# Kernel tuning notes

Measured on AMD Instinct MI355X. Metric: run time of the kernel, lower is better.

Reference implementation:

```python
import jax, jax.numpy as jnp
import numpy as np

N_ATOMS = 200000   # total atoms in batch
N_NBR   = 10       # max neighbors per atom (a2a width)
N_MOLS  = 8000     # molecules in batch (25 atoms each)
HID     = 128      # hidden_size
FDIM    = 151      # raw atom feature dim (GROVER default)
FEAT    = 200      # molecule-level descriptor dim
DFF     = 4 * HID  # PositionwiseFeedForward inner dim
FFN_H   = 256      # mol_atom_from_atom_ffn hidden
TASKS   = 12       # num_tasks
EPS     = 1e-6     # GROVER LayerNorm eps


def setup_inputs() -> dict:
    key = jax.random.key(0)
    ks = jax.random.split(key, 14)
    s = 0.02
    atoms_per_mol = N_ATOMS // N_MOLS
    starts = (jnp.arange(N_MOLS, dtype=jnp.int32) * atoms_per_mol)
    sizes = jnp.full((N_MOLS,), atoms_per_mol, dtype=jnp.int32)
    a_scope = jnp.stack([starts, sizes], axis=1)  # [M, 2]
    return {
        "atom_output": jax.random.normal(ks[0], (N_ATOMS, HID), jnp.float32),
        "original_f_atoms": jax.random.normal(ks[1], (N_ATOMS, FDIM), jnp.float32),
        "features_batch": jax.random.normal(ks[2], (N_MOLS, FEAT), jnp.float32),
        "a2a": jax.random.randint(ks[3], (N_ATOMS, N_NBR), 0, N_ATOMS, jnp.int32),
        "a_scope": a_scope,
        # PositionwiseFeedForward (ffn_atom_from_atom): in = FDIM + HID
        "W1": jax.random.normal(ks[4], (FDIM + HID, DFF), jnp.float32) * s,
        "b1": jnp.zeros((DFF,), jnp.float32),
        "W2": jax.random.normal(ks[5], (DFF, HID), jnp.float32) * s,
        "b2": jnp.zeros((HID,), jnp.float32),
        # SublayerConnection LayerNorm
        "gamma": jnp.ones((HID,), jnp.float32),
        "beta": jnp.zeros((HID,), jnp.float32),
        # mol_atom_from_atom_ffn: in = HID + FEAT
        "Wf1": jax.random.normal(ks[6], (HID + FEAT, FFN_H), jnp.float32) * s,
        "bf1": jnp.zeros((FFN_H,), jnp.float32),
        "Wf2": jax.random.normal(ks[7], (FFN_H, TASKS), jnp.float32) * s,
        "bf2": jnp.zeros((TASKS,), jnp.float32),
    }


def _layernorm(x, gamma, beta):
    mu = jnp.mean(x, axis=-1, keepdims=True)
    var = jnp.mean((x - mu) ** 2, axis=-1, keepdims=True)
    return gamma * (x - mu) * jax.lax.rsqrt(var + EPS) + beta


def reference(atom_output, original_f_atoms, features_batch, a2a, a_scope,
              W1, b1, W2, b2, gamma, beta, Wf1, bf1, Wf2, bf2):
    # select_neighbor_and_aggregate: gather neighbor embeddings, sum over nbrs
    aggr = jnp.sum(atom_output[a2a], axis=1)                      # [N, HID]
    x = jnp.concatenate([original_f_atoms, aggr], axis=1)         # [N, FDIM+HID]
    # PositionwiseFeedForward (eval: dropout = identity)
    h = jax.nn.relu(x @ W1 + b1)
    ffn_out = h @ W2 + b2                                         # [N, HID]
    # SublayerConnection(None, x) -> dropout(LayerNorm(x))
    atom_emb = _layernorm(ffn_out, gamma, beta)                   # [N, HID]
    # Readout: mean-pool per molecule via a_scope (start, size)
    starts = a_scope[:, 0]
    sizes = a_scope[:, 1].astype(atom_emb.dtype)
    seg = jnp.searchsorted(starts, jnp.arange(atom_emb.shape[0], dtype=starts.dtype), side="right") - 1
    mol = jax.ops.segment_sum(atom_emb, seg, num_segments=a_scope.shape[0]) / sizes[:, None]
    # concat molecule descriptors, then mol_atom_from_atom_ffn
    mol = jnp.concatenate([mol, features_batch], axis=1)          # [M, HID+FEAT]
    out = jax.nn.relu(mol @ Wf1 + bf1) @ Wf2 + bf2                # [M, TASKS]
    return out
```

## Files before the change

kernel.cpp:

```cpp
#include <hip/hip_runtime.h>
#include <hip/hip_bf16.h>

#define N_ATOMS 200000
#define N_NBR 10
#define N_MOLS 8000
#define HID 128
#define FDIM 151
#define FEAT 200
#define DFF 512
#define FFN_H 256
#define TASKS 12
#define KX 279
#define K1P 288
#define XSB 288
#define HSB 128
#define FS 132
#define KM 328
#define K3 352
#define MS 360
#define MT 80
#define MI 5
#define SMEM_ATOMS (MT * XSB * 2 + MT * HSB * 2)

typedef __hip_bfloat16 bf16;
typedef __attribute__((ext_vector_type(8))) __bf16 bf16x8;
typedef __attribute__((ext_vector_type(4))) float f32x4;

__device__ __forceinline__ float bf2f(bf16 x) { return __bfloat162float(x); }
__device__ __forceinline__ float blo(unsigned w) { union { unsigned u; float f; } c; c.u = w << 16; return c.f; }
__device__ __forceinline__ float bhi(unsigned w) { union { unsigned u; float f; } c; c.u = w & 0xFFFF0000u; return c.f; }

__device__ __forceinline__ int xswz(int r, int e) {
  return r * XSB + (e ^ ((e < 256 ? (r & 7) : (r & 3)) << 3));
}
__device__ __forceinline__ int hswz(int r, int e) {
  return r * HSB + (e ^ ((r & 7) << 3));
}

__global__ void prep_weights_kernel(const float* __restrict__ W1,
                                    const float* __restrict__ W2,
                                    const float* __restrict__ Wf1,
                                    bf16* __restrict__ W1bT,
                                    bf16* __restrict__ W2bT,
                                    bf16* __restrict__ Wf1bT) {
  int idx = blockIdx.x * 256 + threadIdx.x;
  if (idx < DFF * K1P) {
    int n = idx / K1P, k = idx - n * K1P;
    float v;
    if (k < HID)      v = W1[(size_t)(FDIM + k) * DFF + n];
    else if (k < KX)  v = W1[(size_t)(k - HID) * DFF + n];
    else              v = 0.f;
    W1bT[idx] = __float2bfloat16(v);
    return;
  }
  idx -= DFF * K1P;
  if (idx < HID * DFF) {
    int n = idx / DFF, k = idx - n * DFF;
    W2bT[idx] = __float2bfloat16(W2[(size_t)k * HID + n]);
    return;
  }
  idx -= HID * DFF;
  if (idx < FFN_H * K3) {
    int n = idx / K3, k = idx - n * K3;
    float v = (k < KM) ? Wf1[(size_t)k * FFN_H + n] : 0.f;
    Wf1bT[idx] = __float2bfloat16(v);
  }
}

__global__ void conv_ao_kernel(const float* __restrict__ ao, bf16* __restrict__ ao16) {
  const int idx = blockIdx.x * 256 + threadIdx.x;
  const float4 v0 = *(const float4*)&ao[(size_t)idx * 8];
  const float4 v1 = *(const float4*)&ao[(size_t)idx * 8 + 4];
  union { bf16 h[8]; uint4 u; } pk;
  pk.h[0] = __float2bfloat16(v0.x); pk.h[1] = __float2bfloat16(v0.y);
  pk.h[2] = __float2bfloat16(v0.z); pk.h[3] = __float2bfloat16(v0.w);
  pk.h[4] = __float2bfloat16(v1.x); pk.h[5] = __float2bfloat16(v1.y);
  pk.h[6] = __float2bfloat16(v1.z); pk.h[7] = __float2bfloat16(v1.w);
  *(uint4*)&ao16[(size_t)idx * 8] = pk.u;
}

__global__ __launch_bounds__(256)
void gather_kernel(const bf16* __restrict__ ao16,
                   const int* __restrict__ a2a,
                   bf16* __restrict__ aggr) {
  const int gid = blockIdx.x * 256 + threadIdx.x;
  const int atom = gid >> 4, c8 = gid & 15;
  int idxs[N_NBR];
#pragma unroll
  for (int j = 0; j < N_NBR; ++j) idxs[j] = a2a[atom * N_NBR + j];
  float s[8];
#pragma unroll
  for (int e = 0; e < 8; ++e) s[e] = 0.f;
#pragma unroll
  for (int j = 0; j < N_NBR; ++j) {
    const uint4 u = *(const uint4*)&ao16[(size_t)idxs[j] * HID + c8 * 8];
    s[0] += blo(u.x); s[1] += bhi(u.x);
    s[2] += blo(u.y); s[3] += bhi(u.y);
    s[4] += blo(u.z); s[5] += bhi(u.z);
    s[6] += blo(u.w); s[7] += bhi(u.w);
  }
  union { bf16 h[8]; uint4 u; } pk;
#pragma unroll
  for (int e = 0; e < 8; ++e) pk.h[e] = __float2bfloat16(s[e]);
  *(uint4*)&aggr[(size_t)atom * HID + c8 * 8] = pk.u;
}

__global__ __launch_bounds__(512, 4)
void atoms_kernel(const bf16* __restrict__ aggr,
                  const float* __restrict__ f_atoms,
                  const bf16* __restrict__ W1bT,
                  const float* __restrict__ b1,
                  const bf16* __restrict__ W2bT,
                  const float* __restrict__ b2,
                  const float* __restrict__ gamma,
                  const float* __restrict__ beta,
                  bf16* __restrict__ atom_emb) {
  extern __shared__ char smem[];
  bf16* Xs = (bf16*)smem;
  bf16* Hs = (bf16*)(smem + MT * XSB * 2);
  float* Fs = (float*)smem;

  const int tid = threadIdx.x;
  const int m0 = blockIdx.x * MT;
  const int lane = tid & 63;
  const int w = tid >> 6;
  const int lr = lane & 15;
  const int lk = lane >> 4;

  {
    int q = tid;
#pragma unroll
    for (int p = 0; p < 3; ++p) {
      if (p < 2 || q < MT * 16) {
        const int r = q >> 4, c8 = q & 15;
        *(uint4*)&Xs[r * XSB + ((c8 ^ (r & 7)) << 3)] =
            *(const uint4*)&aggr[(size_t)(m0 + r) * HID + c8 * 8];
      }
      q += 512;
    }
  }
  {
    const float* fb = &f_atoms[(size_t)m0 * FDIM];
    int u = tid;
#pragma unroll
    for (int p = 0; p < 3; ++p) {
      if (p < 2 || u < MT * 19) {
        const int row = u / 19, o = u - row * 19;
        const float* src = &fb[row * FDIM + o * 8];
        float vf[8];
        if (o < 18) {
          const float4 va = *(const float4*)src;
          const float4 vb = *(const float4*)(src + 4);
          vf[0] = va.x; vf[1] = va.y; vf[2] = va.z; vf[3] = va.w;
          vf[4] = vb.x; vf[5] = vb.y; vf[6] = vb.z; vf[7] = vb.w;
        } else {
          const float4 va = *(const float4*)src;
          vf[0] = va.x; vf[1] = va.y; vf[2] = va.z; vf[3] = va.w;
          vf[4] = src[4]; vf[5] = src[5]; vf[6] = src[6]; vf[7] = 0.f;
        }
        union { bf16 h[8]; uint4 q4; } pk;
#pragma unroll
        for (int e = 0; e < 8; ++e) pk.h[e] = __float2bfloat16(vf[e]);
        const int ob = 16 + o;
        const int obs = (ob < 32) ? (ob ^ (row & 7)) : (ob ^ (row & 3));
        *(uint4*)&Xs[row * XSB + obs * 8] = pk.q4;
      }
      u += 512;
    }
  }
  if (tid < MT) {
    const uint4 z = {0u, 0u, 0u, 0u};
    *(uint4*)&Xs[tid * XSB + ((35 ^ (tid & 3)) << 3)] = z;
  }
  __syncthreads();

  f32x4 acc2[MI];
#pragma unroll
  for (int mi = 0; mi < MI; ++mi) acc2[mi] = (f32x4)0.f;

#pragma unroll 1
  for (int pp = 0; pp < 2; ++pp) {
    const int c0 = pp * 2;
    f32x4 acc1[2][MI];
#pragma unroll
    for (int c = 0; c < 2; ++c)
#pragma unroll
      for (int mi = 0; mi < MI; ++mi) acc1[c][mi] = (f32x4)0.f;
    {
      const bf16* w1p = &W1bT[(size_t)(c0 * 128 + w * 16 + lr) * K1P + lk * 8];
      __builtin_amdgcn_s_setprio(1);
#pragma unroll
      for (int kk = 0; kk < K1P / 32; ++kk) {
        const bf16x8 b0 = *(const bf16x8*)&w1p[kk * 32];
        const bf16x8 b1f = *(const bf16x8*)&w1p[(size_t)128 * K1P + kk * 32];
#pragma unroll
        for (int mi = 0; mi < MI; ++mi) {
          const bf16x8 a = *(const bf16x8*)&Xs[xswz(mi * 16 + lr, kk * 32 + lk * 8)];
          acc1[0][mi] = __builtin_amdgcn_mfma_f32_16x16x32_bf16(b0, a, acc1[0][mi], 0, 0, 0);
          acc1[1][mi] = __builtin_amdgcn_mfma_f32_16x16x32_bf16(b1f, a, acc1[1][mi], 0, 0, 0);
        }
      }
      __builtin_amdgcn_s_setprio(0);
    }
#pragma unroll
    for (int c = 0; c < 2; ++c) {
      const int nc = c0 + c;
      {
        const float4 bb = *(const float4*)&b1[nc * 128 + w * 16 + lk * 4];
        const float bbf[4] = { bb.x, bb.y, bb.z, bb.w };
#pragma unroll
        for (int mi = 0; mi < MI; ++mi) {
          union { bf16 h[4]; uint2 u2; } pk;
#pragma unroll
          for (int r = 0; r < 4; ++r) {
            const float h = acc1[c][mi][r] + bbf[r];
            pk.h[r] = __float2bfloat16(h > 0.f ? h : 0.f);
          }
          *(uint2*)&Hs[hswz(mi * 16 + lr, w * 16 + lk * 4)] = pk.u2;
        }
      }
      __syncthreads();
      {
        const bf16* w2p = &W2bT[(size_t)(w * 16 + lr) * DFF + nc * 128 + lk * 8];
        __builtin_amdgcn_s_setprio(1);
#pragma unroll
        for (int kk = 0; kk < 4; ++kk) {
          const bf16x8 wb = *(const bf16x8*)&w2p[kk * 32];
#pragma unroll
          for (int mi = 0; mi < MI; ++mi) {
            const bf16x8 hb = *(const bf16x8*)&Hs[hswz(mi * 16 + lr, kk * 32 + lk * 8)];
            acc2[mi] = __builtin_amdgcn_mfma_f32_16x16x32_bf16(wb, hb, acc2[mi], 0, 0, 0);
          }
        }
        __builtin_amdgcn_s_setprio(0);
      }
      __syncthreads();
    }
  }

  {
    const float4 b2v = *(const float4*)&b2[w * 16 + lk * 4];
#pragma unroll
    for (int mi = 0; mi < MI; ++mi) {
      float4 v;
      v.x = acc2[mi][0] + b2v.x;
      v.y = acc2[mi][1] + b2v.y;
      v.z = acc2[mi][2] + b2v.z;
      v.w = acc2[mi][3] + b2v.w;
      *(float4*)&Fs[(mi * 16 + lr) * FS + w * 16 + lk * 4] = v;
    }
  }
  __syncthreads();

  const float gam0 = gamma[lane], gam1 = gamma[64 + lane];
  const float bet0 = beta[lane],  bet1 = beta[64 + lane];
#pragma unroll
  for (int i = 0; i < MT / 8; ++i) {
    const int row = w * (MT / 8) + i;
    const float x0 = Fs[row * FS + lane];
    const float x1 = Fs[row * FS + 64 + lane];
    float s = x0 + x1;
    float q = x0 * x0 + x1 * x1;
#pragma unroll
    for (int off = 32; off > 0; off >>= 1) {
      s += __shfl_xor(s, off);
      q += __shfl_xor(q, off);
    }
    const float mu = s * (1.f / 128.f);
    const float var = q * (1.f / 128.f) - mu * mu;
    const float rs = rsqrtf(var + 1e-6f);
    const int atom = m0 + row;
    atom_emb[(size_t)atom * HID + lane] =
        __float2bfloat16(gam0 * ((x0 - mu) * rs) + bet0);
    atom_emb[(size_t)atom * HID + 64 + lane] =
        __float2bfloat16(gam1 * ((x1 - mu) * rs) + bet1);
  }
}

__global__ __launch_bounds__(256)
void mol_kernel(const bf16* __restrict__ atom_emb,
                const float* __restrict__ features,
                const int* __restrict__ a_scope,
                bf16* __restrict__ mol_cat) {
  const int tid = threadIdx.x;
  const int mi = tid >> 4, c8 = tid & 15;
  const int base = blockIdx.x * 16;
  const int m = base + mi;
  const int start = a_scope[2 * m];
  const int size  = a_scope[2 * m + 1];
  float s[8];
#pragma unroll
  for (int e = 0; e < 8; ++e) s[e] = 0.f;
  for (int a = 0; a < size; ++a) {
    const uint4 u = *(const uint4*)&atom_emb[(size_t)(start + a) * HID + c8 * 8];
    s[0] += blo(u.x); s[1] += bhi(u.x);
    s[2] += blo(u.y); s[3] += bhi(u.y);
    s[4] += blo(u.z); s[5] += bhi(u.z);
    s[6] += blo(u.w); s[7] += bhi(u.w);
  }
  const float inv = 1.f / (float)size;
  union { bf16 h[8]; uint4 u; } pk;
#pragma unroll
  for (int e = 0; e < 8; ++e) pk.h[e] = __float2bfloat16(s[e] * inv);
  *(uint4*)&mol_cat[(size_t)m * K3 + c8 * 8] = pk.u;
  for (int q = tid; q < 16 * 50; q += 256) {
    const int mm = q / 50, qq = q - mm * 50;
    const float4 v = *(const float4*)&features[(size_t)(base + mm) * FEAT + qq * 4];
    union { bf16 h[4]; uint2 u2; } pf;
    pf.h[0] = __float2bfloat16(v.x); pf.h[1] = __float2bfloat16(v.y);
    pf.h[2] = __float2bfloat16(v.z); pf.h[3] = __float2bfloat16(v.w);
    *(uint2*)&mol_cat[(size_t)(base + mm) * K3 + HID + qq * 4] = pf.u2;
  }
  for (int q = tid; q < 16 * (K3 - KM); q += 256) {
    const int mm = q / (K3 - KM), qq = q - mm * (K3 - KM);
    mol_cat[(size_t)(base + mm) * K3 + KM + qq] = __float2bfloat16(0.f);
  }
}

__global__ __launch_bounds__(512)
void molffn1_kernel(const bf16* __restrict__ mol_cat,
                    const bf16* __restrict__ Wf1bT,
                    const float* __restrict__ bf1,
                    bf16* __restrict__ Hf) {
  __shared__ bf16 As[64 * MS];
  const int tid = threadIdx.x;
  const int m0 = blockIdx.x * 64;
  for (int idx = tid; idx < 64 * (K3 / 8); idx += 512) {
    int rr = idx / (K3 / 8), qv = idx - rr * (K3 / 8);
    *(uint4*)&As[rr * MS + qv * 8] = *(const uint4*)&mol_cat[(size_t)(m0 + rr) * K3 + qv * 8];
  }
  __syncthreads();
  const int lane = tid & 63, w = tid >> 6;
  const int lr = lane & 15, lk = lane >> 4;
  const int wn = w * 32;
  f32x4 acc[4][2];
#pragma unroll
  for (int mi = 0; mi < 4; ++mi)
#pragma unroll
    for (int ni = 0; ni < 2; ++ni) acc[mi][ni] = (f32x4)0.f;
#pragma unroll 3
  for (int kk = 0; kk < K3 / 32; ++kk) {
    bf16x8 a[4], b[2];
#pragma unroll
    for (int mi = 0; mi < 4; ++mi)
      a[mi] = *(const bf16x8*)&As[(mi * 16 + lr) * MS + kk * 32 + lk * 8];
#pragma unroll
    for (int ni = 0; ni < 2; ++ni)
      b[ni] = *(const bf16x8*)&Wf1bT[(size_t)(wn + ni * 16 + lr) * K3 + kk * 32 + lk * 8];
#pragma unroll
    for (int mi = 0; mi < 4; ++mi)
#pragma unroll
      for (int ni = 0; ni < 2; ++ni)
        acc[mi][ni] = __builtin_amdgcn_mfma_f32_16x16x32_bf16(a[mi], b[ni], acc[mi][ni], 0, 0, 0);
  }
#pragma unroll
  for (int ni = 0; ni < 2; ++ni) {
    const int n = wn + ni * 16 + lr;
    const float bias = bf1[n];
#pragma unroll
    for (int mi = 0; mi < 4; ++mi)
#pragma unroll
      for (int rr = 0; rr < 4; ++rr) {
        const int row = mi * 16 + lk * 4 + rr;
        const float h = acc[mi][ni][rr] + bias;
        Hf[(size_t)(m0 + row) * FFN_H + n] = __float2bfloat16(h > 0.f ? h : 0.f);
      }
  }
}

__global__ __launch_bounds__(192)
void molffn2_kernel(const bf16* __restrict__ Hf,
                    const float* __restrict__ Wf2,
                    const float* __restrict__ bias2,
                    float* __restrict__ out) {
  __shared__ float Ws[FFN_H * TASKS];
  const int tid = threadIdx.x;
  for (int i = tid; i < FFN_H * TASKS; i += 192) Ws[i] = Wf2[i];
  __syncthreads();
  const int m = blockIdx.x * 16 + tid / TASKS;
  const int t = tid % TASKS;
  float s = bias2[t];
  for (int k8 = 0; k8 < FFN_H / 8; ++k8) {
    const uint4 u = *(const uint4*)&Hf[(size_t)m * FFN_H + k8 * 8];
    const float h[8] = { blo(u.x), bhi(u.x), blo(u.y), bhi(u.y),
                         blo(u.z), bhi(u.z), blo(u.w), bhi(u.w) };
#pragma unroll
    for (int e = 0; e < 8; ++e) s += h[e] * Ws[(k8 * 8 + e) * TASKS + t];
  }
  out[(size_t)m * TASKS + t] = s;
}

extern "C" void kernel_launch(void* const* d_in, const int* in_sizes, int n_in,
                              void* d_out, int out_size, void* d_ws, size_t ws_size,
                              hipStream_t stream) {
  const float* atom_output = (const float*)d_in[0];
  const float* f_atoms     = (const float*)d_in[1];
  const float* features    = (const float*)d_in[2];
  const int*   a2a         = (const int*)d_in[3];
  const int*   a_scope     = (const int*)d_in[4];
  const float* W1   = (const float*)d_in[5];
  const float* b1   = (const float*)d_in[6];
  const float* W2   = (const float*)d_in[7];
  const float* b2   = (const float*)d_in[8];
  const float* gamma = (const float*)d_in[9];
  const float* beta  = (const float*)d_in[10];
  const float* Wf1  = (const float*)d_in[11];
  const float* bf1  = (const float*)d_in[12];
  const float* Wf2  = (const float*)d_in[13];
  const float* bf2v = (const float*)d_in[14];
  float* out = (float*)d_out;

  char* ws = (char*)d_ws;
  size_t off = 0;
  bf16* W1bT  = (bf16*)(ws + off); off += (size_t)DFF * K1P * 2;
  bf16* W2bT  = (bf16*)(ws + off); off += (size_t)HID * DFF * 2;
  bf16* Wf1bT = (bf16*)(ws + off); off += (size_t)FFN_H * K3 * 2;
  bf16* atom_emb = (bf16*)(ws + off); off += (size_t)N_ATOMS * HID * 2;
  bf16* mol_cat  = (bf16*)(ws + off); off += (size_t)N_MOLS * K3 * 2;
  bf16* Hf       = (bf16*)(ws + off); off += (size_t)N_MOLS * FFN_H * 2;
  bf16* ao16     = (bf16*)(ws + off); off += (size_t)N_ATOMS * HID * 2;
  bf16* aggr = atom_emb;

  hipFuncSetAttribute((const void*)atoms_kernel,
                      hipFuncAttributeMaxDynamicSharedMemorySize, SMEM_ATOMS);

  hipLaunchKernelGGL(prep_weights_kernel, dim3(1184), dim3(256), 0, stream,
                     W1, W2, Wf1, W1bT, W2bT, Wf1bT);
  hipLaunchKernelGGL(conv_ao_kernel, dim3(N_ATOMS * HID / 8 / 256), dim3(256), 0, stream,
                     atom_output, ao16);
  hipLaunchKernelGGL(gather_kernel, dim3(N_ATOMS * 16 / 256), dim3(256), 0, stream,
                     ao16, a2a, aggr);
  hipLaunchKernelGGL(atoms_kernel, dim3(N_ATOMS / MT), dim3(512), SMEM_ATOMS, stream,
                     aggr, f_atoms,
                     W1bT, b1, W2bT, b2, gamma, beta, atom_emb);
  hipLaunchKernelGGL(mol_kernel, dim3(N_MOLS / 16), dim3(256), 0, stream,
                     atom_emb, features, a_scope, mol_cat);
  hipLaunchKernelGGL(molffn1_kernel, dim3(N_MOLS / 64), dim3(512), 0, stream,
                     mol_cat, Wf1bT, bf1, Hf);
  hipLaunchKernelGGL(molffn2_kernel, dim3(N_MOLS / 16), dim3(192), 0, stream,
                     Hf, Wf2, bf2v, out);
}
```

Baseline: 283.6 us.

## Process two atom tiles per block and prefetch next tile's features

The atoms kernel now handles two 80-atom tiles per block, halving the grid. While the first tile's GEMMs run, the second tile's f_atoms rows are loaded into registers, hiding that global load latency. The first GEMM is restructured to compute one 128-column chunk at a time instead of two, which lowers register pressure at the cost of more barriers and fewer independent MFMA chains. A custom barrier waits only on LDS counters, so the outstanding global prefetch is not drained; the halved grid may worsen tail imbalance across CUs.

```diff
diff --git a/kernel.cpp b/kernel.cpp
--- a/kernel.cpp
+++ b/kernel.cpp
@@ -26,6 +26,8 @@
 typedef __attribute__((ext_vector_type(8))) __bf16 bf16x8;
 typedef __attribute__((ext_vector_type(4))) float f32x4;
 
+#define BAR() do { asm volatile("s_waitcnt lgkmcnt(0)" ::: "memory"); __builtin_amdgcn_s_barrier(); } while (0)
+
 __device__ __forceinline__ float bf2f(bf16 x) { return __bfloat162float(x); }
 __device__ __forceinline__ float blo(unsigned w) { union { unsigned u; float f; } c; c.u = w << 16; return c.f; }
 __device__ __forceinline__ float bhi(unsigned w) { union { unsigned u; float f; } c; c.u = w & 0xFFFF0000u; return c.f; }
@@ -121,90 +123,110 @@
   float* Fs = (float*)smem;
 
   const int tid = threadIdx.x;
-  const int m0 = blockIdx.x * MT;
   const int lane = tid & 63;
   const int w = tid >> 6;
   const int lr = lane & 15;
   const int lk = lane >> 4;
+  const int urow = tid / 19;
+  const int uo = tid - urow * 19;
+
+  float4 fa0[3], fa1[3];
 
   {
-    int q = tid;
-#pragma unroll
-    for (int p = 0; p < 3; ++p) {
-      if (p < 2 || q < MT * 16) {
-        const int r = q >> 4, c8 = q & 15;
-        *(uint4*)&Xs[r * XSB + ((c8 ^ (r & 7)) << 3)] =
-            *(const uint4*)&aggr[(size_t)(m0 + r) * HID + c8 * 8];
-      }
-      q += 512;
-    }
-  }
-  {
-    const float* fb = &f_atoms[(size_t)m0 * FDIM];
+    const float* fb = &f_atoms[(size_t)(blockIdx.x * 2) * MT * FDIM];
     int u = tid;
 #pragma unroll
     for (int p = 0; p < 3; ++p) {
       if (p < 2 || u < MT * 19) {
-        const int row = u / 19, o = u - row * 19;
+        const int row = u / 19, o = u - (u / 19) * 19;
         const float* src = &fb[row * FDIM + o * 8];
-        float vf[8];
-        if (o < 18) {
-          const float4 va = *(const float4*)src;
-          const float4 vb = *(const float4*)(src + 4);
-          vf[0] = va.x; vf[1] = va.y; vf[2] = va.z; vf[3] = va.w;
-          vf[4] = vb.x; vf[5] = vb.y; vf[6] = vb.z; vf[7] = vb.w;
-        } else {
-          const float4 va = *(const float4*)src;
-          vf[0] = va.x; vf[1] = va.y; vf[2] = va.z; vf[3] = va.w;
-          vf[4] = src[4]; vf[5] = src[5]; vf[6] = src[6]; vf[7] = 0.f;
-        }
-        union { bf16 h[8]; uint4 q4; } pk;
-#pragma unroll
-        for (int e = 0; e < 8; ++e) pk.h[e] = __float2bfloat16(vf[e]);
-        const int ob = 16 + o;
-        const int obs = (ob < 32) ? (ob ^ (row & 7)) : (ob ^ (row & 3));
-        *(uint4*)&Xs[row * XSB + obs * 8] = pk.q4;
+        fa0[p] = *(const float4*)src;
+        if (o < 18) fa1[p] = *(const float4*)(src + 4);
+        else { fa1[p].x = src[4]; fa1[p].y = src[5]; fa1[p].z = src[6]; fa1[p].w = 0.f; }
       }
       u += 512;
     }
   }
-  if (tid < MT) {
-    const uint4 z = {0u, 0u, 0u, 0u};
-    *(uint4*)&Xs[tid * XSB + ((35 ^ (tid & 3)) << 3)] = z;
-  }
-  __syncthreads();
-
-  f32x4 acc2[MI];
-#pragma unroll
-  for (int mi = 0; mi < MI; ++mi) acc2[mi] = (f32x4)0.f;
+
+#pragma unroll
+  for (int t = 0; t < 2; ++t) {
+    const int m0 = (blockIdx.x * 2 + t) * MT;
+
+    {
+      int q = tid;
+#pragma unroll
+      for (int p = 0; p < 3; ++p) {
+        if (p < 2 || q < MT * 16) {
+          const int r = q >> 4, c8 = q & 15;
+          *(uint4*)&Xs[r * XSB + ((c8 ^ (r & 7)) << 3)] =
+              *(const uint4*)&aggr[(size_t)(m0 + r) * HID + c8 * 8];
+        }
+        q += 512;
+      }
+    }
+    {
+      int u = tid;
+#pragma unroll
+      for (int p = 0; p < 3; ++p) {
+        if (p < 2 || u < MT * 19) {
+          const int row = u / 19, o = u - (u / 19) * 19;
+          const float vf[8] = { fa0[p].x, fa0[p].y, fa0[p].z, fa0[p].w,
+                                fa1[p].x, fa1[p].y, fa1[p].z, fa1[p].w };
+          union { bf16 h[8]; uint4 q4; } pk;
+#pragma unroll
+          for (int e = 0; e < 8; ++e) pk.h[e] = __float2bfloat16(vf[e]);
+          const int ob = 16 + o;
+          const int obs = (ob < 32) ? (ob ^ (row & 7)) : (ob ^ (row & 3));
+          *(uint4*)&Xs[row * XSB + obs * 8] = pk.q4;
+        }
+        u += 512;
+      }
+    }
+    if (tid < MT) {
+      const uint4 z = {0u, 0u, 0u, 0u};
+      *(uint4*)&Xs[tid * XSB + ((35 ^ (tid & 3)) << 3)] = z;
+    }
+    BAR();
+
+    if (t == 0) {
+      const float* fb = &f_atoms[(size_t)(blockIdx.x * 2 + 1) * MT * FDIM];
+      int u = tid;
+#pragma unroll
+      for (int p = 0; p < 3; ++p) {
+        if (p < 2 || u < MT * 19) {
+          const int row = u / 19, o = u - (u / 19) * 19;
+          const float* src = &fb[row * FDIM + o * 8];
+          fa0[p] = *(const float4*)src;
+          if (o < 18) fa1[p] = *(const float4*)(src + 4);
+          else { fa1[p].x = src[4]; fa1[p].y = src[5]; fa1[p].z = src[6]; fa1[p].w = 0.f; }
+        }
+        u += 512;
+      }
+    }
+
+    f32x4 acc2[MI];
+#pragma unroll
+    for (int mi = 0; mi < MI; ++mi) acc2[mi] = (f32x4)0.f;
 
 #pragma unroll 1
-  for (int pp = 0; pp < 2; ++pp) {
-    const int c0 = pp * 2;
-    f32x4 acc1[2][MI];
-#pragma unroll
-    for (int c = 0; c < 2; ++c)
-#pragma unroll
-      for (int mi = 0; mi < MI; ++mi) acc1[c][mi] = (f32x4)0.f;
-    {
-      const bf16* w1p = &W1bT[(size_t)(c0 * 128 + w * 16 + lr) * K1P + lk * 8];
-      __builtin_amdgcn_s_setprio(1);
-#pragma unroll
-      for (int kk = 0; kk < K1P / 32; ++kk) {
-        const bf16x8 b0 = *(const bf16x8*)&w1p[kk * 32];
-        const bf16x8 b1f = *(const bf16x8*)&w1p[(size_t)128 * K1P + kk * 32];
-#pragma unroll
-        for (int mi = 0; mi < MI; ++mi) {
-          const bf16x8 a = *(const bf16x8*)&Xs[xswz(mi * 16 + lr, kk * 32 + lk * 8)];
-          acc1[0][mi] = __builtin_amdgcn_mfma_f32_16x16x32_bf16(b0, a, acc1[0][mi], 0, 0, 0);
-          acc1[1][mi] = __builtin_amdgcn_mfma_f32_16x16x32_bf16(b1f, a, acc1[1][mi], 0, 0, 0);
-        }
-      }
-      __builtin_amdgcn_s_setprio(0);
-    }
-#pragma unroll
-    for (int c = 0; c < 2; ++c) {
-      const int nc = c0 + c;
+    for (int nc = 0; nc < 4; ++nc) {
+      f32x4 acc1[MI];
+#pragma unroll
+      for (int mi = 0; mi < MI; ++mi) acc1[mi] = (f32x4)0.f;
+      {
+        const bf16* w1p = &W1bT[(size_t)(nc * 128 + w * 16 + lr) * K1P + lk * 8];
+        __builtin_amdgcn_s_setprio(1);
+#pragma unroll
+        for (int kk = 0; kk < K1P / 32; ++kk) {
+          const bf16x8 b0 = *(const bf16x8*)&w1p[kk * 32];
+#pragma unroll
+          for (int mi = 0; mi < MI; ++mi) {
+            const bf16x8 a = *(const bf16x8*)&Xs[xswz(mi * 16 + lr, kk * 32 + lk * 8)];
+            acc1[mi] = __builtin_amdgcn_mfma_f32_16x16x32_bf16(b0, a, acc1[mi], 0, 0, 0);
+          }
+        }
+        __builtin_amdgcn_s_setprio(0);
+      }
       {
         const float4 bb = *(const float4*)&b1[nc * 128 + w * 16 + lk * 4];
         const float bbf[4] = { bb.x, bb.y, bb.z, bb.w };
@@ -213,13 +235,13 @@
           union { bf16 h[4]; uint2 u2; } pk;
 #pragma unroll
           for (int r = 0; r < 4; ++r) {
-            const float h = acc1[c][mi][r] + bbf[r];
+            const float h = acc1[mi][r] + bbf[r];
             pk.h[r] = __float2bfloat16(h > 0.f ? h : 0.f);
           }
           *(uint2*)&Hs[hswz(mi * 16 + lr, w * 16 + lk * 4)] = pk.u2;
         }
       }
-      __syncthreads();
+      BAR();
       {
         const bf16* w2p = &W2bT[(size_t)(w * 16 + lr) * DFF + nc * 128 + lk * 8];
         __builtin_amdgcn_s_setprio(1);
@@ -234,47 +256,49 @@
         }
         __builtin_amdgcn_s_setprio(0);
       }
-      __syncthreads();
-    }
-  }
-
-  {
-    const float4 b2v = *(const float4*)&b2[w * 16 + lk * 4];
-#pragma unroll
-    for (int mi = 0; mi < MI; ++mi) {
-      float4 v;
-      v.x = acc2[mi][0] + b2v.x;
-      v.y = acc2[mi][1] + b2v.y;
-      v.z = acc2[mi][2] + b2v.z;
-      v.w = acc2[mi][3] + b2v.w;
-      *(float4*)&Fs[(mi * 16 + lr) * FS + w * 16 + lk * 4] = v;
-    }
-  }
-  __syncthreads();
-
-  const float gam0 = gamma[lane], gam1 = gamma[64 + lane];
-  const float bet0 = beta[lane],  bet1 = beta[64 + lane];
-#pragma unroll
-  for (int i = 0; i < MT / 8; ++i) {
-    const int row = w * (MT / 8) + i;
-    const float x0 = Fs[row * FS + lane];
-    const float x1 = Fs[row * FS + 64 + lane];
-    float s = x0 + x1;
-    float q = x0 * x0 + x1 * x1;
-#pragma unroll
-    for (int off = 32; off > 0; off >>= 1) {
-      s += __shfl_xor(s, off);
-      q += __shfl_xor(q, off);
-    }
-    const float mu = s * (1.f / 128.f);
-    const float var = q * (1.f / 128.f) - mu * mu;
-    const float rs = rsqrtf(var + 1e-6f);
-    const int atom = m0 + row;
-    atom_emb[(size_t)atom * HID + lane] =
-        __float2bfloat16(gam0 * ((x0 - mu) * rs) + bet0);
-    atom_emb[(size_t)atom * HID + 64 + lane] =
-        __float2bfloat16(gam1 * ((x1 - mu) * rs) + bet1);
-  }
+      BAR();
+    }
+
+    {
+      const float4 b2v = *(const float4*)&b2[w * 16 + lk * 4];
+#pragma unroll
+      for (int mi = 0; mi < MI; ++mi) {
+        float4 v;
+        v.x = acc2[mi][0] + b2v.x;
+        v.y = acc2[mi][1] + b2v.y;
+        v.z = acc2[mi][2] + b2v.z;
+        v.w = acc2[mi][3] + b2v.w;
+        *(float4*)&Fs[(mi * 16 + lr) * FS + w * 16 + lk * 4] = v;
+      }
+    }
+    BAR();
+
+    const float gam0 = gamma[lane], gam1 = gamma[64 + lane];
+    const float bet0 = beta[lane],  bet1 = beta[64 + lane];
+#pragma unroll
+    for (int i = 0; i < MT / 8; ++i) {
+      const int row = w * (MT / 8) + i;
+      const float x0 = Fs[row * FS + lane];
+      const float x1 = Fs[row * FS + 64 + lane];
+      float s = x0 + x1;
+      float q = x0 * x0 + x1 * x1;
+#pragma unroll
+      for (int off = 32; off > 0; off >>= 1) {
+        s += __shfl_xor(s, off);
+        q += __shfl_xor(q, off);
+      }
+      const float mu = s * (1.f / 128.f);
+      const float var = q * (1.f / 128.f) - mu * mu;
+      const float rs = rsqrtf(var + 1e-6f);
+      const int atom = m0 + row;
+      atom_emb[(size_t)atom * HID + lane] =
+          __float2bfloat16(gam0 * ((x0 - mu) * rs) + bet0);
+      atom_emb[(size_t)atom * HID + 64 + lane] =
+          __float2bfloat16(gam1 * ((x1 - mu) * rs) + bet1);
+    }
+    if (t == 0) BAR();
+  }
+  (void)urow; (void)uo;
 }
 
 __global__ __launch_bounds__(256)
@@ -430,7 +454,7 @@
                      atom_output, ao16);
   hipLaunchKernelGGL(gather_kernel, dim3(N_ATOMS * 16 / 256), dim3(256), 0, stream,
                      ao16, a2a, aggr);
-  hipLaunchKernelGGL(atoms_kernel, dim3(N_ATOMS / MT), dim3(512), SMEM_ATOMS, stream,
+  hipLaunchKernelGGL(atoms_kernel, dim3(N_ATOMS / MT / 2), dim3(512), SMEM_ATOMS, stream,
                      aggr, f_atoms,
                      W1bT, b1, W2bT, b2, gamma, beta, atom_emb);
   hipLaunchKernelGGL(mol_kernel, dim3(N_MOLS / 16), dim3(256), 0, stream,
```

Measured after the change: 316.3 us. +11.5%, slower.
